# Kernel tuning notes

Hardware: AMD Instinct MI355X
Metric: run time of the kernel (lower is better)

The kernel has to match this reference:

```python
import jax, jax.numpy as jnp
import numpy as np

N = 100000   # nodes
E = 1600000  # edges
G = 64       # graphs in batch
H, C = 8, 16 # heads, per-head channels
HID = H * C  # 128
EMB, BBOX, TOK, REL = 256, 32, 151, 51
IN0 = EMB + BBOX  # 288
NEG_SLOPE = 0.2
BN_EPS = 1e-5


def setup_inputs() -> dict:
    key = jax.random.key(0)
    ks = jax.random.split(key, 32)
    f = lambda i, shape: jax.random.normal(ks[i], shape, dtype=jnp.float32) * 0.05
    inp = {}
    inp["tok_id"] = jax.random.randint(ks[0], (N,), 0, TOK)
    inp["bbox"] = jax.random.normal(ks[1], (N, 4), dtype=jnp.float32)
    inp["edge_index"] = jax.random.randint(ks[2], (2, E), 0, N)
    inp["edge_attr"] = jax.random.randint(ks[3], (E,), 0, REL)
    inp["batch"] = jnp.sort(jax.random.randint(ks[4], (N,), 0, G))
    inp["tok_emb"] = f(5, (TOK, EMB))
    inp["bbox_W"] = f(6, (4, BBOX)); inp["bbox_b"] = f(7, (BBOX,))
    inp["rel_emb"] = f(8, (REL, C))
    # layer 0 (in_dim 288 -> 128)
    inp["Wl0"] = f(9, (IN0, HID));  inp["bl0"] = f(10, (HID,))
    inp["Wr0"] = f(11, (IN0, HID)); inp["br0"] = f(12, (HID,))
    inp["We0"] = f(13, (C, HID));   inp["att0"] = f(14, (H, C))
    inp["bias0"] = f(15, (HID,))
    inp["gamma0"] = jnp.ones((HID,), jnp.float32); inp["beta0"] = jnp.zeros((HID,), jnp.float32)
    # layers 1..2 stacked (128 -> 128)
    inp["WlS"] = f(16, (2, HID, HID)); inp["blS"] = f(17, (2, HID))
    inp["WrS"] = f(18, (2, HID, HID)); inp["brS"] = f(19, (2, HID))
    inp["WeS"] = f(20, (2, C, HID));   inp["attS"] = f(21, (2, H, C))
    inp["biasS"] = f(22, (2, HID))
    inp["gammaS"] = jnp.ones((2, HID), jnp.float32); inp["betaS"] = jnp.zeros((2, HID), jnp.float32)
    return inp


def gatv2_layer(x, src, dst, e_emb, Wl, bl, Wr, br, We, att, bias):
    """GATv2Conv: gather -> leaky_relu attention -> segment softmax -> scatter."""
    xl = (x @ Wl + bl).reshape(-1, H, C)   # source transform [N,H,C]
    xr = (x @ Wr + br).reshape(-1, H, C)   # target transform [N,H,C]
    ee = (e_emb @ We).reshape(-1, H, C)    # edge transform  [E,H,C]
    m = jax.nn.leaky_relu(xl[src] + xr[dst] + ee, NEG_SLOPE)  # [E,H,C]
    logits = jnp.einsum('ehc,hc->eh', m, att)                 # [E,H]
    amax = jax.ops.segment_max(logits, dst, num_segments=N)   # [N,H]
    p = jnp.exp(logits - amax[dst])
    denom = jax.ops.segment_sum(p, dst, num_segments=N)       # [N,H]
    alpha = p / jnp.maximum(denom[dst], 1e-16)                # [E,H]
    out = jax.ops.segment_sum(alpha[..., None] * xl[src], dst, num_segments=N)  # [N,H,C]
    return out.reshape(-1, HID) + bias


def batch_norm(x, gamma, beta):
    mu = jnp.mean(x, axis=0)
    var = jnp.var(x, axis=0)
    return gamma * (x - mu) * jax.lax.rsqrt(var + BN_EPS) + beta


def reference(tok_id, bbox, edge_index, edge_attr, batch,
              tok_emb, bbox_W, bbox_b, rel_emb,
              Wl0, bl0, Wr0, br0, We0, att0, bias0, gamma0, beta0,
              WlS, blS, WrS, brS, WeS, attS, biasS, gammaS, betaS):
    src, dst = edge_index[0], edge_index[1]
    x = jnp.concatenate([tok_emb[tok_id], bbox @ bbox_W + bbox_b], axis=-1)  # [N,288]
    e_emb = rel_emb[edge_attr]  # [E,16]
    h = batch_norm(jax.nn.relu(
        gatv2_layer(x, src, dst, e_emb, Wl0, bl0, Wr0, br0, We0, att0, bias0)),
        gamma0, beta0)
    for i in range(2):
        h = h + batch_norm(jax.nn.relu(
            gatv2_layer(h, src, dst, e_emb, WlS[i], blS[i], WrS[i], brS[i], WeS[i], attS[i], biasS[i])),
            gammaS[i], betaS[i])
    # global mean pool over graphs
    sums = jax.ops.segment_sum(h, batch, num_segments=G)
    counts = jax.ops.segment_sum(jnp.ones((h.shape[0],), h.dtype), batch, num_segments=G)
    return sums / jnp.maximum(counts, 1.0)[:, None]  # [G,128]
```

## Files before the change

### kernel.cpp

```cpp
#include <hip/hip_runtime.h>

#define N_NODES 100000
#define N_PAD   100096
#define N_EDGES 1600000
#define NGRAPH  64
#define NHEAD   8
#define NCH     16
#define HID     128
#define IN0     288
#define NREL    51
#define EMB     256
#define NBBOX   32
#define NEG_SLOPE 0.2f
#define EPS_BN  1e-5f
#define AGG_BLOCKS 2048
#define POOL_BLOCKS 1024
#define SENT 0x03F00000u
#define SENT_MIN ((uint)(NREL) << 20)
#define L2E 1.4426950408889634f

typedef unsigned int uint;
typedef unsigned short ushort;

typedef __bf16 bf16_t;
typedef bf16_t bfx8 __attribute__((ext_vector_type(8)));
typedef float  fx4  __attribute__((ext_vector_type(4)));
typedef float  v2f  __attribute__((ext_vector_type(2)));

__device__ __forceinline__ ushort f2bf(float f) {
  uint u = __float_as_uint(f);
  u += 0x7fffu + ((u >> 16) & 1u);
  return (ushort)(u >> 16);
}
__device__ __forceinline__ float bf2f(uint u) { return __uint_as_float(u << 16); }
__device__ __forceinline__ v2f up2(uint u) {
  v2f r;
  r.x = __uint_as_float(u << 16);
  r.y = __uint_as_float(u & 0xffff0000u);
  return r;
}
__device__ __forceinline__ void unpack8(uint4 u, float* f) {
  f[0] = __uint_as_float(u.x << 16); f[1] = __uint_as_float(u.x & 0xffff0000u);
  f[2] = __uint_as_float(u.y << 16); f[3] = __uint_as_float(u.y & 0xffff0000u);
  f[4] = __uint_as_float(u.z << 16); f[5] = __uint_as_float(u.z & 0xffff0000u);
  f[6] = __uint_as_float(u.w << 16); f[7] = __uint_as_float(u.w & 0xffff0000u);
}

__global__ void se_prep(const float* __restrict__ Wl0, const float* __restrict__ Wr0,
                        const float* __restrict__ WlS, const float* __restrict__ WrS,
                        const float* __restrict__ rel_emb, const float* __restrict__ We0,
                        const float* __restrict__ WeS,
                        const float* __restrict__ bl0, const float* __restrict__ br0,
                        const float* __restrict__ blS, const float* __restrict__ brS,
                        ushort* __restrict__ W0T, ushort* __restrict__ WST,
                        float* __restrict__ eetab, float* __restrict__ biascat) {
  int i = blockIdx.x * 256 + threadIdx.x;
  if (i < 256 * IN0) {
    int j = i / IN0, k = i - j * IN0;
    float v = (j < 128) ? Wl0[k * 128 + j] : Wr0[k * 128 + (j - 128)];
    W0T[j * IN0 + k] = f2bf(v);
    return;
  }
  i -= 256 * IN0;
  if (i < 2 * 256 * HID) {
    int li = i >> 15;
    int rem = i & 32767;
    int j = rem >> 7, k = rem & 127;
    float v = (j < 128) ? WlS[(li * 128 + k) * 128 + j] : WrS[(li * 128 + k) * 128 + (j - 128)];
    WST[(li * 256 + j) * 128 + k] = f2bf(v);
    return;
  }
  i -= 2 * 256 * HID;
  if (i < 3 * NREL * HID) {
    int li = i / (NREL * HID);
    int rem = i - li * (NREL * HID);
    int r = rem >> 7, j = rem & 127;
    const float* We = (li == 0) ? We0 : (WeS + (li - 1) * NCH * HID);
    float s = 0.f;
#pragma unroll
    for (int c = 0; c < NCH; c++) s += rel_emb[r * NCH + c] * We[c * HID + j];
    eetab[li * (NREL * HID) + rem] = s;
    return;
  }
  i -= 3 * NREL * HID;
  if (i < 3 * 256) {
    int li = i >> 8, j = i & 255;
    const float* bl = (li == 0) ? bl0 : (blS + (li - 1) * HID);
    const float* br = (li == 0) ? br0 : (brS + (li - 1) * HID);
    biascat[i] = (j < 128) ? bl[j] : br[j - 128];
  }
}

__global__ void se_build_x(const int* __restrict__ tok_id, const float* __restrict__ bbox,
                           const float* __restrict__ tok_emb, const float* __restrict__ bbox_W,
                           const float* __restrict__ bbox_b, ushort* __restrict__ x) {
  int idx = blockIdx.x * 256 + threadIdx.x;
  if (idx >= N_PAD * 36) return;
  int n = idx / 36, c = (idx - n * 36) * 8;
  float f[8];
  if (n >= N_NODES) {
#pragma unroll
    for (int j = 0; j < 8; j++) f[j] = 0.f;
  } else if (c < EMB) {
    const float* te = tok_emb + (size_t)tok_id[n] * EMB + c;
    const float4 t0 = *(const float4*)te, t1 = *(const float4*)(te + 4);
    f[0] = t0.x; f[1] = t0.y; f[2] = t0.z; f[3] = t0.w;
    f[4] = t1.x; f[5] = t1.y; f[6] = t1.z; f[7] = t1.w;
  } else {
    const int j0 = c - EMB;
    const float4 bb = *(const float4*)(bbox + (size_t)n * 4);
#pragma unroll
    for (int j = 0; j < 8; j++) {
      float v = bbox_b[j0 + j];
      v += bb.x * bbox_W[0 * NBBOX + j0 + j];
      v += bb.y * bbox_W[1 * NBBOX + j0 + j];
      v += bb.z * bbox_W[2 * NBBOX + j0 + j];
      v += bb.w * bbox_W[3 * NBBOX + j0 + j];
      f[j] = v;
    }
  }
  uint4 p;
  p.x = ((uint)f2bf(f[1]) << 16) | f2bf(f[0]);
  p.y = ((uint)f2bf(f[3]) << 16) | f2bf(f[2]);
  p.z = ((uint)f2bf(f[5]) << 16) | f2bf(f[4]);
  p.w = ((uint)f2bf(f[7]) << 16) | f2bf(f[6]);
  ((uint4*)x)[idx] = p;
}

__global__ void se_hist(const int* __restrict__ ei, int* __restrict__ deg) {
  int e = blockIdx.x * 256 + threadIdx.x;
  if (e < N_EDGES) atomicAdd(&deg[ei[N_EDGES + e]], 1);
}
__global__ __launch_bounds__(1024) void se_scanA(const int* __restrict__ deg,
                                                 int* __restrict__ offs, int* __restrict__ bsum) {
  __shared__ int s[1024];
  const int tid = threadIdx.x;
  const int i = blockIdx.x * 1024 + tid;
  int v = (i < N_NODES) ? ((deg[i] + 3) & ~3) : 0;
  s[tid] = v;
  __syncthreads();
  for (int d = 1; d < 1024; d <<= 1) {
    int t = (tid >= d) ? s[tid - d] : 0;
    __syncthreads();
    s[tid] += t;
    __syncthreads();
  }
  if (i < N_NODES) offs[i] = s[tid] - v;
  if (tid == 1023) bsum[blockIdx.x] = s[1023];
}
__global__ __launch_bounds__(128) void se_scanB(int* __restrict__ bsum, int nb) {
  __shared__ int s[128];
  const int t = threadIdx.x;
  int v = (t < nb) ? bsum[t] : 0;
  s[t] = v;
  __syncthreads();
  for (int d = 1; d < 128; d <<= 1) {
    int u = (t >= d) ? s[t - d] : 0;
    __syncthreads();
    s[t] += u;
    __syncthreads();
  }
  if (t < nb) bsum[t] = s[t] - v;
}
__global__ __launch_bounds__(1024) void se_scanC(int* __restrict__ offs, const int* __restrict__ bsum) {
  int i = blockIdx.x * 1024 + threadIdx.x;
  if (i < N_NODES) offs[i] += bsum[blockIdx.x];
}
__global__ void se_padfill(const int* __restrict__ deg, const int* __restrict__ offs,
                           uint* __restrict__ csrp) {
  int n = blockIdx.x * 256 + threadIdx.x;
  if (n >= N_NODES) return;
  const int d = deg[n];
  const int s = offs[n] + d;
  const int c = ((d + 3) & ~3) - d;
  for (int j = 0; j < c; j++) csrp[s + j] = SENT;
}
__global__ void se_scatter(const int* __restrict__ ei, const int* __restrict__ eattr,
                           const int* __restrict__ offs, int* __restrict__ cur,
                           uint* __restrict__ csrp) {
  int e = blockIdx.x * 256 + threadIdx.x;
  if (e < N_EDGES) {
    int d = ei[N_EDGES + e];
    int p = offs[d] + atomicAdd(&cur[d], 1);
    csrp[p] = (uint)ei[e] | ((uint)eattr[e] << 20);
  }
}

template <int K>
__global__ __launch_bounds__(256) void se_gemm(const ushort* __restrict__ A,
                                               const ushort* __restrict__ BT,
                                               const float* __restrict__ bias,
                                               ushort* __restrict__ C) {
  __shared__ __align__(16) ushort As[128 * 32];
  __shared__ __align__(16) ushort Bs[128 * 32];
  const int tid = threadIdx.x;
  const int w = tid >> 6, l = tid & 63;
  const int wr = w >> 1, wc = w & 1;
  const int m0 = blockIdx.x * 128, n0 = blockIdx.y * 128;
  fx4 acc[4][4];
#pragma unroll
  for (int i = 0; i < 4; i++)
#pragma unroll
    for (int j = 0; j < 4; j++) acc[i][j] = fx4{0.f, 0.f, 0.f, 0.f};

  for (int k0 = 0; k0 < K; k0 += 32) {
#pragma unroll
    for (int ch = 0; ch < 2; ch++) {
      const int t = tid + ch * 256;
      const int r = t >> 2, c = (t & 3) << 3;
      const ushort* ga = A + (size_t)(m0 + r) * K + (k0 + c);
      ushort* la = As + (size_t)(ch * 256 + w * 64) * 8;
      __builtin_amdgcn_global_load_lds((const __attribute__((address_space(1))) void*)ga,
                                       (__attribute__((address_space(3))) void*)la, 16, 0, 0);
      const ushort* gb = BT + (size_t)(n0 + r) * K + (k0 + c);
      ushort* lb = Bs + (size_t)(ch * 256 + w * 64) * 8;
      __builtin_amdgcn_global_load_lds((const __attribute__((address_space(1))) void*)gb,
                                       (__attribute__((address_space(3))) void*)lb, 16, 0, 0);
    }
    __syncthreads();
    bfx8 af[4], bfr[4];
#pragma unroll
    for (int i = 0; i < 4; i++) {
      af[i]  = *(const bfx8*)(As + ((wr * 64 + i * 16 + (l & 15)) * 32 + ((l >> 4) * 8)));
      bfr[i] = *(const bfx8*)(Bs + ((wc * 64 + i * 16 + (l & 15)) * 32 + ((l >> 4) * 8)));
    }
#pragma unroll
    for (int i = 0; i < 4; i++)
#pragma unroll
      for (int j = 0; j < 4; j++)
        acc[i][j] = __builtin_amdgcn_mfma_f32_16x16x32_bf16(af[i], bfr[j], acc[i][j], 0, 0, 0);
    __syncthreads();
  }
#pragma unroll
  for (int i = 0; i < 4; i++) {
    const int rbase = m0 + wr * 64 + i * 16 + ((l >> 4) << 2);
#pragma unroll
    for (int j = 0; j < 4; j++) {
      const int col = n0 + wc * 64 + j * 16 + (l & 15);
      const float bz = bias[col];
#pragma unroll
      for (int r2 = 0; r2 < 4; r2++) {
        const int row = rbase + r2;
        if (row < N_NODES) C[(size_t)row * 256 + col] = f2bf(acc[i][j][r2] + bz);
      }
    }
  }
}

__global__ __launch_bounds__(256) void se_agg(const uint4* __restrict__ xlxr4,
                                              const uint* __restrict__ csrp,
                                              const int* __restrict__ offs, const int* __restrict__ deg,
                                              const float* __restrict__ eetab,
                                              const float* __restrict__ att,
                                              const float* __restrict__ bias,
                                              float* __restrict__ y, float* __restrict__ partial) {
  __shared__ ushort ee[64 * HID];
  __shared__ float bstat[256];
  const int tid = threadIdx.x, w = tid >> 6, l = tid & 63;
  const int g = l >> 4, k = l & 15;
  for (int i = tid; i < 64 * HID; i += 256) {
    const int r = i >> 7;
    ee[i] = (r < NREL) ? f2bf(eetab[i]) : (ushort)0;
  }
  bstat[tid] = 0.f;
  __syncthreads();
  v2f av[4], bv[4];
  {
    const float* ap = att + (k >> 1) * NCH + (k & 1) * 8;
    const float* bp = bias + k * 8;
#pragma unroll
    for (int q = 0; q < 4; q++) {
      av[q] = v2f{ap[2 * q] * L2E, ap[2 * q + 1] * L2E};
      bv[q] = v2f{bp[2 * q], bp[2 * q + 1]};
    }
  }
  v2f sv[4], qv[4];
#pragma unroll
  for (int q = 0; q < 4; q++) { sv[q] = v2f{0.f, 0.f}; qv[q] = v2f{0.f, 0.f}; }
  const v2f zero = v2f{0.f, 0.f};

  const int stride = gridDim.x * 4;
  for (int n = blockIdx.x * 4 + w; n < N_NODES; n += stride) {
    const int rs = offs[n];
    const int nit = (deg[n] + 3) >> 2;
    v2f xrv[4];
    {
      const uint4 xru = xlxr4[(uint)n * 32u + 16u + (uint)k];
      xrv[0] = up2(xru.x); xrv[1] = up2(xru.y); xrv[2] = up2(xru.z); xrv[3] = up2(xru.w);
    }
    float den = 0.f;
    v2f acc[4];
#pragma unroll
    for (int q = 0; q < 4; q++) acc[q] = zero;

    uint eA = SENT, eB = SENT;
    uint4 xlv = uint4{0u, 0u, 0u, 0u};
    if (nit > 0) {
      eA = csrp[rs + g];
      xlv = xlxr4[(eA & 0xFFFFFu) * 32u + (uint)k];
      if (nit > 1) eB = csrp[rs + 4 + g];
    }
    for (int i = 0; i < nit; ++i) {
      const uint ec = eA;
      const uint4 xc = xlv;
      eA = eB;
      if (i + 1 < nit) xlv = xlxr4[(eA & 0xFFFFFu) * 32u + (uint)k];
      if (i + 2 < nit) eB = csrp[rs + 4 * (i + 2) + g];
      const uint rel = ec >> 20;
      const uint4 eeu = *(const uint4*)(ee + rel * HID + k * 8);
      v2f xls[4];
      v2f sd = zero;
      {
        const uint xcu[4] = {xc.x, xc.y, xc.z, xc.w};
        const uint eu[4] = {eeu.x, eeu.y, eeu.z, eeu.w};
#pragma unroll
        for (int q = 0; q < 4; q++) {
          const v2f xl = up2(xcu[q]);
          v2f m = xl + xrv[q] + up2(eu[q]);
          const v2f lk = __builtin_elementwise_max(m, zero) +
                         NEG_SLOPE * __builtin_elementwise_min(m, zero);
          sd += lk * av[q];
          xls[q] = xl;
        }
      }
      float s = sd.x + sd.y;
      s += __shfl_xor(s, 1);
      s = (ec >= SENT_MIN) ? -1e30f : s;
      const float p = exp2f(s);
      den += p;
      const v2f pp = v2f{p, p};
#pragma unroll
      for (int q = 0; q < 4; q++) acc[q] += pp * xls[q];
    }
    den += __shfl_xor(den, 16);
    den += __shfl_xor(den, 32);
#pragma unroll
    for (int q = 0; q < 4; q++) {
      acc[q].x += __shfl_xor(acc[q].x, 16); acc[q].x += __shfl_xor(acc[q].x, 32);
      acc[q].y += __shfl_xor(acc[q].y, 16); acc[q].y += __shfl_xor(acc[q].y, 32);
    }
    if (g == 0) {
      const float r = 1.f / fmaxf(den, 1e-16f);
      const v2f rr = v2f{r, r};
      v2f ov[4];
#pragma unroll
      for (int q = 0; q < 4; q++) {
        ov[q] = __builtin_elementwise_max(acc[q] * rr + bv[q], zero);
        sv[q] += ov[q];
        qv[q] += ov[q] * ov[q];
      }
      float4* yp = (float4*)y + (size_t)n * 32 + (size_t)k * 2;
      yp[0] = make_float4(ov[0].x, ov[0].y, ov[1].x, ov[1].y);
      yp[1] = make_float4(ov[2].x, ov[2].y, ov[3].x, ov[3].y);
    }
  }
  if (l < 16) {
#pragma unroll
    for (int q = 0; q < 4; q++) {
      unsafeAtomicAdd(&bstat[k * 8 + 2 * q], sv[q].x);
      unsafeAtomicAdd(&bstat[k * 8 + 2 * q + 1], sv[q].y);
      unsafeAtomicAdd(&bstat[128 + k * 8 + 2 * q], qv[q].x);
      unsafeAtomicAdd(&bstat[128 + k * 8 + 2 * q + 1], qv[q].y);
    }
  }
  __syncthreads();
  partial[(size_t)tid * AGG_BLOCKS + blockIdx.x] = bstat[tid];
}

__global__ __launch_bounds__(256) void se_stats(const float* __restrict__ partial, float* __restrict__ musig) {
  __shared__ float red[256];
  const int ch = blockIdx.x, tid = threadIdx.x;
  float s = 0.f;
  for (int i = tid; i < AGG_BLOCKS; i += 256) s += partial[ch * AGG_BLOCKS + i];
  red[tid] = s; __syncthreads();
  for (int o = 128; o > 0; o >>= 1) { if (tid < o) red[tid] += red[tid + o]; __syncthreads(); }
  const float sum = red[0]; __syncthreads();
  float q = 0.f;
  for (int i = tid; i < AGG_BLOCKS; i += 256) q += partial[(128 + ch) * AGG_BLOCKS + i];
  red[tid] = q; __syncthreads();
  for (int o = 128; o > 0; o >>= 1) { if (tid < o) red[tid] += red[tid + o]; __syncthreads(); }
  if (tid == 0) {
    const float mean = sum / (float)N_NODES;
    const float var = red[0] / (float)N_NODES - mean * mean;
    musig[ch] = mean;
    musig[128 + ch] = rsqrtf(var + EPS_BN);
  }
}

__global__ void se_bn(const float* __restrict__ y, const float* __restrict__ musig,
                      const float* __restrict__ gamma, const float* __restrict__ beta,
                      ushort* __restrict__ h_bf, int residual) {
  int idx = blockIdx.x * 256 + threadIdx.x;
  if (idx >= N_NODES * 16) return;
  const int k = idx & 15;
  const float4 y0 = ((const float4*)y)[(size_t)idx * 2];
  const float4 y1 = ((const float4*)y)[(size_t)idx * 2 + 1];
  const float4 mu0 = ((const float4*)musig)[k * 2],         mu1 = ((const float4*)musig)[k * 2 + 1];
  const float4 rs0 = ((const float4*)(musig + 128))[k * 2], rs1 = ((const float4*)(musig + 128))[k * 2 + 1];
  const float4 g0  = ((const float4*)gamma)[k * 2],         g1  = ((const float4*)gamma)[k * 2 + 1];
  const float4 b0  = ((const float4*)beta)[k * 2],          b1  = ((const float4*)beta)[k * 2 + 1];
  float v[8];
  v[0] = g0.x * (y0.x - mu0.x) * rs0.x + b0.x;
  v[1] = g0.y * (y0.y - mu0.y) * rs0.y + b0.y;
  v[2] = g0.z * (y0.z - mu0.z) * rs0.z + b0.z;
  v[3] = g0.w * (y0.w - mu0.w) * rs0.w + b0.w;
  v[4] = g1.x * (y1.x - mu1.x) * rs1.x + b1.x;
  v[5] = g1.y * (y1.y - mu1.y) * rs1.y + b1.y;
  v[6] = g1.z * (y1.z - mu1.z) * rs1.z + b1.z;
  v[7] = g1.w * (y1.w - mu1.w) * rs1.w + b1.w;
  if (residual) {
    const uint4 ho = ((const uint4*)h_bf)[idx];
    float f[8];
    unpack8(ho, f);
#pragma unroll
    for (int j = 0; j < 8; j++) v[j] += f[j];
  }
  uint4 p4;
  p4.x = ((uint)f2bf(v[1]) << 16) | f2bf(v[0]);
  p4.y = ((uint)f2bf(v[3]) << 16) | f2bf(v[2]);
  p4.z = ((uint)f2bf(v[5]) << 16) | f2bf(v[4]);
  p4.w = ((uint)f2bf(v[7]) << 16) | f2bf(v[6]);
  ((uint4*)h_bf)[idx] = p4;
}

__global__ __launch_bounds__(256) void se_pool(const ushort* __restrict__ h_bf,
                                               const int* __restrict__ batch,
                                               float* __restrict__ pool) {
  const int tid = threadIdx.x, w = tid >> 6, l = tid & 63;
  const int wid = blockIdx.x * 4 + w;
  const int nw = gridDim.x * 4;
  const int chunk = (N_NODES + nw - 1) / nw;
  const int start = wid * chunk;
  const int end = min(N_NODES, start + chunk);
  float a0 = 0.f, a1 = 0.f;
  int cg = -1, cnt = 0;
  for (int n = start; n < end; ++n) {
    const int gg = batch[n];
    if (gg != cg) {
      if (cg >= 0) {
        unsafeAtomicAdd(&pool[cg * HID + 2 * l], a0);
        unsafeAtomicAdd(&pool[cg * HID + 2 * l + 1], a1);
        if (l == 0) unsafeAtomicAdd(&pool[NGRAPH * HID + cg], (float)cnt);
      }
      a0 = 0.f; a1 = 0.f; cnt = 0; cg = gg;
    }
    const uint u = ((const uint*)h_bf)[(size_t)n * 64 + l];
    a0 += bf2f(u & 0xffffu);
    a1 += __uint_as_float(u & 0xffff0000u);
    cnt++;
  }
  if (cg >= 0) {
    unsafeAtomicAdd(&pool[cg * HID + 2 * l], a0);
    unsafeAtomicAdd(&pool[cg * HID + 2 * l + 1], a1);
    if (l == 0) unsafeAtomicAdd(&pool[NGRAPH * HID + cg], (float)cnt);
  }
}
__global__ void se_poolfin(const float* __restrict__ pool, float* __restrict__ out) {
  int idx = blockIdx.x * 256 + threadIdx.x;
  if (idx < NGRAPH * HID) {
    int g = idx >> 7;
    out[idx] = pool[idx] / fmaxf(pool[NGRAPH * HID + g], 1.f);
  }
}

extern "C" void kernel_launch(void* const* d_in, const int* in_sizes, int n_in,
                              void* d_out, int out_size, void* d_ws, size_t ws_size,
                              hipStream_t stream) {
  (void)in_sizes; (void)n_in; (void)out_size; (void)ws_size;
  const int*   tok_id  = (const int*)d_in[0];
  const float* bbox    = (const float*)d_in[1];
  const int*   ei      = (const int*)d_in[2];
  const int*   eattr   = (const int*)d_in[3];
  const int*   batch   = (const int*)d_in[4];
  const float* tok_emb = (const float*)d_in[5];
  const float* bbox_W  = (const float*)d_in[6];
  const float* bbox_b  = (const float*)d_in[7];
  const float* rel_emb = (const float*)d_in[8];
  const float* Wl0  = (const float*)d_in[9];
  const float* bl0  = (const float*)d_in[10];
  const float* Wr0  = (const float*)d_in[11];
  const float* br0  = (const float*)d_in[12];
  const float* We0  = (const float*)d_in[13];
  const float* att0 = (const float*)d_in[14];
  const float* bias0  = (const float*)d_in[15];
  const float* gamma0 = (const float*)d_in[16];
  const float* beta0  = (const float*)d_in[17];
  const float* WlS  = (const float*)d_in[18];
  const float* blS  = (const float*)d_in[19];
  const float* WrS  = (const float*)d_in[20];
  const float* brS  = (const float*)d_in[21];
  const float* WeS  = (const float*)d_in[22];
  const float* attS = (const float*)d_in[23];
  const float* biasS  = (const float*)d_in[24];
  const float* gammaS = (const float*)d_in[25];
  const float* betaS  = (const float*)d_in[26];
  float* out = (float*)d_out;

  char* ws = (char*)d_ws;
  size_t off = 0;
  auto alloc = [&](size_t bytes) -> char* {
    char* p = ws + off;
    off = (off + bytes + 255) & ~(size_t)255;
    return p;
  };
  ushort* x_bf = (ushort*)alloc((size_t)N_PAD * IN0 * 2);
  float*  y    = (float*)x_bf;
  ushort* xlxr = (ushort*)alloc((size_t)N_PAD * 256 * 2);
  ushort* h_bf = (ushort*)alloc((size_t)N_PAD * HID * 2);
  ushort* W0T  = (ushort*)alloc((size_t)256 * IN0 * 2);
  ushort* WST  = (ushort*)alloc((size_t)2 * 256 * HID * 2);
  float*  eetab   = (float*)alloc((size_t)3 * NREL * HID * 4);
  float*  biascat = (float*)alloc((size_t)3 * 256 * 4);
  int* deg  = (int*)alloc((size_t)N_NODES * 4);
  int* offs = (int*)alloc((size_t)(N_NODES + 1) * 4);
  int* cur  = (int*)alloc((size_t)N_NODES * 4);
  int* bsum = (int*)alloc(128 * 4);
  uint* csrp = (uint*)alloc((size_t)(N_EDGES + 3 * N_NODES + 256) * 4);
  float* partial = (float*)alloc((size_t)256 * AGG_BLOCKS * 4);
  float* musig   = (float*)alloc(256 * 4);
  float* pool    = (float*)alloc((size_t)(NGRAPH * HID + NGRAPH) * 4);

  hipMemsetAsync(deg, 0, (size_t)N_NODES * 4, stream);
  hipMemsetAsync(cur, 0, (size_t)N_NODES * 4, stream);
  hipMemsetAsync(pool, 0, (size_t)(NGRAPH * HID + NGRAPH) * 4, stream);

  se_prep<<<624, 256, 0, stream>>>(Wl0, Wr0, WlS, WrS, rel_emb, We0, WeS,
                                   bl0, br0, blS, brS, W0T, WST, eetab, biascat);
  se_build_x<<<(N_PAD * 36 + 255) / 256, 256, 0, stream>>>(tok_id, bbox, tok_emb, bbox_W, bbox_b, x_bf);
  se_hist<<<(N_EDGES + 255) / 256, 256, 0, stream>>>(ei, deg);
  se_scanA<<<98, 1024, 0, stream>>>(deg, offs, bsum);
  se_scanB<<<1, 128, 0, stream>>>(bsum, 98);
  se_scanC<<<98, 1024, 0, stream>>>(offs, bsum);
  se_padfill<<<(N_NODES + 255) / 256, 256, 0, stream>>>(deg, offs, csrp);
  se_scatter<<<(N_EDGES + 255) / 256, 256, 0, stream>>>(ei, eattr, offs, cur, csrp);

  se_gemm<IN0><<<dim3(N_PAD / 128, 2), 256, 0, stream>>>(x_bf, W0T, biascat, xlxr);
  se_agg<<<AGG_BLOCKS, 256, 0, stream>>>((const uint4*)xlxr, csrp, offs, deg,
                                         eetab, att0, bias0, y, partial);
  se_stats<<<128, 256, 0, stream>>>(partial, musig);
  se_bn<<<(N_NODES * 16 + 255) / 256, 256, 0, stream>>>(y, musig, gamma0, beta0, h_bf, 0);

  for (int li = 0; li < 2; ++li) {
    se_gemm<HID><<<dim3(N_PAD / 128, 2), 256, 0, stream>>>(h_bf, WST + (size_t)li * 256 * HID,
                                                           biascat + (li + 1) * 256, xlxr);
    se_agg<<<AGG_BLOCKS, 256, 0, stream>>>((const uint4*)xlxr, csrp, offs, deg,
                                           eetab + (size_t)(li + 1) * NREL * HID,
                                           attS + (size_t)li * NHEAD * NCH,
                                           biasS + (size_t)li * HID, y, partial);
    se_stats<<<128, 256, 0, stream>>>(partial, musig);
    se_bn<<<(N_NODES * 16 + 255) / 256, 256, 0, stream>>>(y, musig, gammaS + (size_t)li * HID,
                                                          betaS + (size_t)li * HID, h_bf, 1);
  }

  se_pool<<<POOL_BLOCKS, 256, 0, stream>>>(h_bf, batch, pool);
  se_poolfin<<<32, 256, 0, stream>>>(pool, out);
}
```

Before: 864.1 us.

## Deepen edge gather prefetch, pack row info, rewrite leaky-relu as abs form

The aggregation kernel now keeps three source-row gathers in flight instead of one. It loads them without guards, relying on 64 extra sentinel entries padded after the last CSR row so the reads past the end stay in bounds. Row offset and iteration count are packed into one int2 array written by the padfill kernel, which replaces two separate loads. Leaky ReLU is rewritten as 0.6*m + 0.4*|m|, folded into two scaled attention vectors, and the bias load moves into the epilogue to free registers. The deeper prefetch raises register pressure and issues redundant gathers of sentinel node 0 at row ends.

```diff
diff --git a/kernel.cpp b/kernel.cpp
--- a/kernel.cpp
+++ b/kernel.cpp
@@ -167,13 +167,19 @@
   if (i < N_NODES) offs[i] += bsum[blockIdx.x];
 }
 __global__ void se_padfill(const int* __restrict__ deg, const int* __restrict__ offs,
-                           uint* __restrict__ csrp) {
+                           uint* __restrict__ csrp, int2* __restrict__ rowinfo) {
   int n = blockIdx.x * 256 + threadIdx.x;
   if (n >= N_NODES) return;
   const int d = deg[n];
-  const int s = offs[n] + d;
+  const int o = offs[n];
+  rowinfo[n] = make_int2(o, (d + 3) >> 2);
+  const int s = o + d;
   const int c = ((d + 3) & ~3) - d;
   for (int j = 0; j < c; j++) csrp[s + j] = SENT;
+  if (n == N_NODES - 1) {
+    const int e = o + ((d + 3) & ~3);
+    for (int j = 0; j < 64; j++) csrp[e + j] = SENT;
+  }
 }
 __global__ void se_scatter(const int* __restrict__ ei, const int* __restrict__ eattr,
                            const int* __restrict__ offs, int* __restrict__ cur,
@@ -249,7 +255,7 @@
 
 __global__ __launch_bounds__(256) void se_agg(const uint4* __restrict__ xlxr4,
                                               const uint* __restrict__ csrp,
-                                              const int* __restrict__ offs, const int* __restrict__ deg,
+                                              const int2* __restrict__ rowinfo,
                                               const float* __restrict__ eetab,
                                               const float* __restrict__ att,
                                               const float* __restrict__ bias,
@@ -264,14 +270,13 @@
   }
   bstat[tid] = 0.f;
   __syncthreads();
-  v2f av[4], bv[4];
+  v2f a1v[4], a2v[4];
   {
     const float* ap = att + (k >> 1) * NCH + (k & 1) * 8;
-    const float* bp = bias + k * 8;
 #pragma unroll
     for (int q = 0; q < 4; q++) {
-      av[q] = v2f{ap[2 * q] * L2E, ap[2 * q + 1] * L2E};
-      bv[q] = v2f{bp[2 * q], bp[2 * q + 1]};
+      a1v[q] = v2f{ap[2 * q] * (0.6f * L2E), ap[2 * q + 1] * (0.6f * L2E)};
+      a2v[q] = v2f{ap[2 * q] * (0.4f * L2E), ap[2 * q + 1] * (0.4f * L2E)};
     }
   }
   v2f sv[4], qv[4];
@@ -281,8 +286,9 @@
 
   const int stride = gridDim.x * 4;
   for (int n = blockIdx.x * 4 + w; n < N_NODES; n += stride) {
-    const int rs = offs[n];
-    const int nit = (deg[n] + 3) >> 2;
+    const int2 ri = rowinfo[n];
+    const uint* rowp = csrp + ri.x + g;
+    const int nit = ri.y;
     v2f xrv[4];
     {
       const uint4 xru = xlxr4[(uint)n * 32u + 16u + (uint)k];
@@ -293,44 +299,37 @@
 #pragma unroll
     for (int q = 0; q < 4; q++) acc[q] = zero;
 
-    uint eA = SENT, eB = SENT;
-    uint4 xlv = uint4{0u, 0u, 0u, 0u};
-    if (nit > 0) {
-      eA = csrp[rs + g];
-      xlv = xlxr4[(eA & 0xFFFFFu) * 32u + (uint)k];
-      if (nit > 1) eB = csrp[rs + 4 + g];
-    }
+    uint e0 = rowp[0], e1 = rowp[4], e2 = rowp[8];
+    uint4 x0 = xlxr4[(e0 & 0xFFFFFu) * 32u + (uint)k];
+    uint4 x1 = xlxr4[(e1 & 0xFFFFFu) * 32u + (uint)k];
+    uint4 x2 = xlxr4[(e2 & 0xFFFFFu) * 32u + (uint)k];
     for (int i = 0; i < nit; ++i) {
-      const uint ec = eA;
-      const uint4 xc = xlv;
-      eA = eB;
-      if (i + 1 < nit) xlv = xlxr4[(eA & 0xFFFFFu) * 32u + (uint)k];
-      if (i + 2 < nit) eB = csrp[rs + 4 * (i + 2) + g];
-      const uint rel = ec >> 20;
-      const uint4 eeu = *(const uint4*)(ee + rel * HID + k * 8);
+      const uint e3 = rowp[4 * i + 12];
+      const uint4 eeu = *(const uint4*)(ee + (e0 >> 20) * HID + k * 8);
+      v2f sd1 = zero, sd2 = zero;
       v2f xls[4];
-      v2f sd = zero;
       {
-        const uint xcu[4] = {xc.x, xc.y, xc.z, xc.w};
+        const uint xcu[4] = {x0.x, x0.y, x0.z, x0.w};
         const uint eu[4] = {eeu.x, eeu.y, eeu.z, eeu.w};
 #pragma unroll
         for (int q = 0; q < 4; q++) {
           const v2f xl = up2(xcu[q]);
-          v2f m = xl + xrv[q] + up2(eu[q]);
-          const v2f lk = __builtin_elementwise_max(m, zero) +
-                         NEG_SLOPE * __builtin_elementwise_min(m, zero);
-          sd += lk * av[q];
+          const v2f m = xl + xrv[q] + up2(eu[q]);
+          sd1 += m * a1v[q];
+          sd2 += __builtin_elementwise_abs(m) * a2v[q];
           xls[q] = xl;
         }
       }
-      float s = sd.x + sd.y;
+      float s = sd1.x + sd1.y + sd2.x + sd2.y;
       s += __shfl_xor(s, 1);
-      s = (ec >= SENT_MIN) ? -1e30f : s;
+      s = (e0 >= SENT_MIN) ? -1e30f : s;
       const float p = exp2f(s);
       den += p;
       const v2f pp = v2f{p, p};
 #pragma unroll
       for (int q = 0; q < 4; q++) acc[q] += pp * xls[q];
+      e0 = e1; x0 = x1; e1 = e2; x1 = x2; e2 = e3;
+      x2 = xlxr4[(e2 & 0xFFFFFu) * 32u + (uint)k];
     }
     den += __shfl_xor(den, 16);
     den += __shfl_xor(den, 32);
@@ -342,6 +341,9 @@
     if (g == 0) {
       const float r = 1.f / fmaxf(den, 1e-16f);
       const v2f rr = v2f{r, r};
+      const float4 b0 = ((const float4*)bias)[k * 2];
+      const float4 b1 = ((const float4*)bias)[k * 2 + 1];
+      const v2f bv[4] = {v2f{b0.x, b0.y}, v2f{b0.z, b0.w}, v2f{b1.x, b1.y}, v2f{b1.z, b1.w}};
       v2f ov[4];
 #pragma unroll
       for (int q = 0; q < 4; q++) {
@@ -515,6 +517,7 @@
   int* offs = (int*)alloc((size_t)(N_NODES + 1) * 4);
   int* cur  = (int*)alloc((size_t)N_NODES * 4);
   int* bsum = (int*)alloc(128 * 4);
+  int2* rowinfo = (int2*)alloc((size_t)N_NODES * 8);
   uint* csrp = (uint*)alloc((size_t)(N_EDGES + 3 * N_NODES + 256) * 4);
   float* partial = (float*)alloc((size_t)256 * AGG_BLOCKS * 4);
   float* musig   = (float*)alloc(256 * 4);
@@ -531,11 +534,11 @@
   se_scanA<<<98, 1024, 0, stream>>>(deg, offs, bsum);
   se_scanB<<<1, 128, 0, stream>>>(bsum, 98);
   se_scanC<<<98, 1024, 0, stream>>>(offs, bsum);
-  se_padfill<<<(N_NODES + 255) / 256, 256, 0, stream>>>(deg, offs, csrp);
+  se_padfill<<<(N_NODES + 255) / 256, 256, 0, stream>>>(deg, offs, csrp, rowinfo);
   se_scatter<<<(N_EDGES + 255) / 256, 256, 0, stream>>>(ei, eattr, offs, cur, csrp);
 
   se_gemm<IN0><<<dim3(N_PAD / 128, 2), 256, 0, stream>>>(x_bf, W0T, biascat, xlxr);
-  se_agg<<<AGG_BLOCKS, 256, 0, stream>>>((const uint4*)xlxr, csrp, offs, deg,
+  se_agg<<<AGG_BLOCKS, 256, 0, stream>>>((const uint4*)xlxr, csrp, rowinfo,
                                          eetab, att0, bias0, y, partial);
   se_stats<<<128, 256, 0, stream>>>(partial, musig);
   se_bn<<<(N_NODES * 16 + 255) / 256, 256, 0, stream>>>(y, musig, gamma0, beta0, h_bf, 0);
@@ -543,7 +546,7 @@
   for (int li = 0; li < 2; ++li) {
     se_gemm<HID><<<dim3(N_PAD / 128, 2), 256, 0, stream>>>(h_bf, WST + (size_t)li * 256 * HID,
                                                            biascat + (li + 1) * 256, xlxr);
-    se_agg<<<AGG_BLOCKS, 256, 0, stream>>>((const uint4*)xlxr, csrp, offs, deg,
+    se_agg<<<AGG_BLOCKS, 256, 0, stream>>>((const uint4*)xlxr, csrp, rowinfo,
                                            eetab + (size_t)(li + 1) * NREL * HID,
                                            attS + (size_t)li * NHEAD * NCH,
                                            biasS + (size_t)li * HID, y, partial);
```

Result: slower. 966.2 us (+11.8%).
